# Optimization experiments

Hardware: AMD Instinct MI355X
Metric: run time of the kernel (lower is better)

The kernel has to match this reference:

```python
import jax, jax.numpy as jnp
import numpy as np

# ---- static config (from init_kwargs) ----
SAMPLE_RATE = 2048.0
MAX_SHIFT = int(0.025 * SAMPLE_RATE)          # 51 samples
NUM_BINS = 16
FFTLENGTH = 1.0                               # chisq_kernel_length (s)
DF = 1.0 / FFTLENGTH
NUM_FREQS = int(FFTLENGTH * SAMPLE_RATE // 2 + 1)   # 1025 == rfft bins of 2048 samples
HIGHPASS = 32.0
CHISQ_PENALTY = 1.0
_freqs = np.arange(NUM_FREQS) / FFTLENGTH
MASK = _freqs >= HIGHPASS                     # static numpy bool mask

BATCH, CHANNELS, DIM = 256, 2, 2048


def setup_inputs() -> dict:
    key = jax.random.key(0)
    k1, k2 = jax.random.split(key)
    x_hat = jax.random.normal(k1, (BATCH, CHANNELS, DIM), dtype=jnp.float32)
    x = jax.random.normal(k2, (BATCH, CHANNELS, DIM), dtype=jnp.float32)
    return {"x_hat": x_hat, "x": x}


def _center(x):
    xmin = x.min(-1, keepdims=True)
    xmax = x.max(-1, keepdims=True)
    return 2 * (x - xmin) / (xmax - xmin) - 1


def _shifted_pearson(x, y, max_shift):
    # x, y: [B, C, T]; returns corr: [W, B, C] with W = 2*max_shift + 1
    b, c, t = x.shape
    num_windows = 2 * max_shift + 1
    xp = jnp.pad(x, ((0, 0), (0, 0), (max_shift, max_shift)))
    # window w, position i -> xp[..., i + w]  (same layout as torch unfold)
    idx = jnp.arange(num_windows)[:, None] + jnp.arange(t)[None, :]   # [W, T]
    xw = xp[:, :, idx]                                                # [B, C, W, T]
    xw = jnp.transpose(xw, (2, 0, 1, 3))                              # [W, B, C, T]
    xw = xw - xw.mean(-1, keepdims=True)
    yc = y - y.mean(-1, keepdims=True)
    corr = (xw * yc).sum(-1)
    norm = (xw ** 2).sum(-1) * (yc ** 2).sum(-1)
    return corr / jnp.sqrt(norm)


def _snr_integral(a, b):
    # |4 * a * conj(b) * df| cumulatively summed over frequency
    integrand = a * jnp.conj(b)
    return jnp.abs(4 * integrand * DF).cumsum(-1)


def _chisq(htilde, stilde):
    htilde = htilde[:, :, MASK]
    stilde = stilde[:, :, MASK]
    # partition frequencies by the template's own optimal-SNR integral
    si = _snr_integral(htilde, htilde)                    # [B, C, F]
    total = si[:, :, -1:]
    bins = (jnp.arange(NUM_BINS + 1, dtype=si.dtype) / NUM_BINS) * total  # [B, C, NB+1]
    search = jax.vmap(jax.vmap(lambda a, v: jnp.searchsorted(a, v, side="right")))
    edges = search(si, bins)
    edges = jnp.clip(edges, 0, si.shape[-1] - 1)
    qtilde = htilde / jnp.sqrt(total).astype(htilde.dtype)
    # SNR per bin of the normalized template against the strain
    si2 = _snr_integral(qtilde, stilde)                   # [B, C, F]
    total2 = si2[:, :, -1:]
    right = jnp.take_along_axis(si2, edges[:, :, 1:], axis=-1)
    left = jnp.take_along_axis(si2, edges[:, :, :-1], axis=-1)
    snr_per_bin = right - left                            # [B, C, NB]
    summand = (snr_per_bin - total2 / NUM_BINS) ** 2
    chisq = NUM_BINS * summand.sum(-1) / (NUM_BINS - 1)
    return total2[:, :, 0], chisq


def reference(x_hat, x):
    x_hat = _center(x_hat)
    corr = _shifted_pearson(x_hat, x, MAX_SHIFT)          # [W, B, C]
    corr = corr.max(0)                                    # [B, C]
    loss = (1 - corr) / (1 + corr)
    htilde = jnp.fft.rfft(x_hat, axis=-1) / SAMPLE_RATE   # [B, C, 1025] complex
    stilde = jnp.fft.rfft(x, axis=-1) / SAMPLE_RATE
    _, chisq = _chisq(htilde, stilde)
    chisq = chisq * CHISQ_PENALTY
    loss = loss * (1 + chisq ** 3) ** (1.0 / 6.0)
    return loss
```

## Files before the change

### kernel.cpp

```cpp
#include <hip/hip_runtime.h>
#include <math.h>

#define ROWS 512
#define DIM 2048
#define MS 51
#define NWIN 103
#define KMIN 32
#define NMASK 993

__global__ __launch_bounds__(512) void fused_mfl_kernel(
    const float* __restrict__ xhat, const float* __restrict__ x,
    float* __restrict__ out)
{
    const int r = blockIdx.x;
    const int t = threadIdx.x;
    const int lane = t & 63;
    const int wave = t >> 6;

    __shared__ float smem[12928];
    float2* A2  = (float2*)smem;
    float2* B2  = (float2*)(smem + 4096);
    float2* TW  = (float2*)(smem + 8192);
    float* eArr = smem + 9216;
    float* gArr = smem + 10240;
    float* red6 = smem + 9216;
    float* ah   = smem + 12288;
    float* xhd  = smem + 12339;
    float* at_  = smem + 12390;
    float* xt_  = smem + 12441;
    float* Ah   = smem + 12492;
    float* Aqh  = smem + 12544;
    float* Xh   = smem + 12596;
    float* At   = smem + 12648;
    float* Aqt  = smem + 12700;
    float* Xt   = smem + 12752;
    float* corrv= smem + 12804;
    float* siA  = smem;
    float* siBr = smem + 1024;

    __shared__ float sc[8];
    __shared__ int   edges[17];
    __shared__ float summ[16];
    __shared__ float wsA[4], wsB[4];

    const float* xhp = xhat + (size_t)r * DIM;
    const float* xrp = x    + (size_t)r * DIM;
    float4 a4 = ((const float4*)xhp)[t];
    float4 b4 = ((const float4*)xrp)[t];
    float av[4] = {a4.x, a4.y, a4.z, a4.w};
    float bv[4] = {b4.x, b4.y, b4.z, b4.w};

    {
        float swv, cwv;
        sincosf((float)t * (-3.14159265358979323846f / 1024.0f), &swv, &cwv);
        TW[t] = make_float2(cwv, swv);
    }

#pragma unroll
    for (int j = 0; j < 4; ++j) {
        int i = 4 * t + j;
        A2[i] = make_float2(av[j], bv[j]);
        if (i < MS)        { ah[i] = av[j]; xhd[i] = bv[j]; }
        if (i >= DIM - MS) { at_[i-(DIM-MS)] = av[j]; xt_[i-(DIM-MS)] = bv[j]; }
    }
    {
        float mn4 = fminf(fminf(av[0],av[1]), fminf(av[2],av[3]));
        float mx4 = fmaxf(fmaxf(av[0],av[1]), fmaxf(av[2],av[3]));
        float sa = (av[0]+av[1])+(av[2]+av[3]);
        float qa = (av[0]*av[0]+av[1]*av[1])+(av[2]*av[2]+av[3]*av[3]);
        float sx = (bv[0]+bv[1])+(bv[2]+bv[3]);
        float qx = (bv[0]*bv[0]+bv[1]*bv[1])+(bv[2]*bv[2]+bv[3]*bv[3]);
        red6[t] = mn4; red6[512+t] = mx4; red6[1024+t] = sa;
        red6[1536+t] = qa; red6[2048+t] = sx; red6[2560+t] = qx;
    }
    __syncthreads();

    auto fft2048 = [&](const float2* Sp, float2* Dp, const int s) {
        const int q = t;
        const int u = q & ~(s - 1);
        float2 x0 = Sp[q], x1 = Sp[q+512], x2 = Sp[q+1024], x3 = Sp[q+1536];
        float t0r=x0.x+x2.x, t0i=x0.y+x2.y;
        float t1r=x0.x-x2.x, t1i=x0.y-x2.y;
        float t2r=x1.x+x3.x, t2i=x1.y+x3.y;
        float d3r=x1.x-x3.x, d3i=x1.y-x3.y;
        float t3r=d3i, t3i=-d3r;
        float2 w1 = TW[u];
        float w2r=w1.x*w1.x-w1.y*w1.y, w2i=2.f*w1.x*w1.y;
        float w3r=w2r*w1.x-w2i*w1.y,  w3i=w2r*w1.y+w2i*w1.x;
        float y0r=t0r+t2r, y0i=t0i+t2i;
        float a1r=t1r+t3r, a1i=t1i+t3i;
        float y1r=a1r*w1.x-a1i*w1.y, y1i=a1r*w1.y+a1i*w1.x;
        float a2r=t0r-t2r, a2i=t0i-t2i;
        float y2r=a2r*w2r-a2i*w2i, y2i=a2r*w2i+a2i*w2r;
        float a3r=t1r-t3r, a3i=t1i-t3i;
        float y3r=a3r*w3r-a3i*w3i, y3i=a3r*w3i+a3i*w3r;
        int base = q + 3*u;
        Dp[base]       = make_float2(y0r,y0i);
        Dp[base+s]     = make_float2(y1r,y1i);
        Dp[base+2*s]   = make_float2(y2r,y2i);
        Dp[base+3*s]   = make_float2(y3r,y3i);
    };
    auto fft1024 = [&](const float2* Sp, float2* Dp, const int s) {
        const int q = t;
        const int u = q & ~(s - 1);
        float2 x0 = Sp[q], x1 = Sp[q+256], x2 = Sp[q+512], x3 = Sp[q+768];
        float t0r=x0.x+x2.x, t0i=x0.y+x2.y;
        float t1r=x0.x-x2.x, t1i=x0.y-x2.y;
        float t2r=x1.x+x3.x, t2i=x1.y+x3.y;
        float d3r=x1.x-x3.x, d3i=x1.y-x3.y;
        float t3r=d3i, t3i=-d3r;
        float2 w1 = TW[2*u];
        float w2r=w1.x*w1.x-w1.y*w1.y, w2i=2.f*w1.x*w1.y;
        float w3r=w2r*w1.x-w2i*w1.y,  w3i=w2r*w1.y+w2i*w1.x;
        float y0r=t0r+t2r, y0i=t0i+t2i;
        float a1r=t1r+t3r, a1i=t1i+t3i;
        float y1r=a1r*w1.x-a1i*w1.y, y1i=a1r*w1.y+a1i*w1.x;
        float a2r=t0r-t2r, a2i=t0i-t2i;
        float y2r=a2r*w2r-a2i*w2i, y2i=a2r*w2i+a2i*w2r;
        float a3r=t1r-t3r, a3i=t1i-t3i;
        float y3r=a3r*w3r-a3i*w3i, y3i=a3r*w3i+a3i*w3r;
        int base = q + 3*u;
        Dp[base]       = make_float2(y0r,y0i);
        Dp[base+s]     = make_float2(y1r,y1i);
        Dp[base+2*s]   = make_float2(y2r,y2i);
        Dp[base+3*s]   = make_float2(y3r,y3i);
    };

    fft2048(A2, B2, 1);
    if (wave == 0) {
        float4 u, v;
        u=((const float4*)(red6     ))[2*lane]; v=((const float4*)(red6     ))[2*lane+1];
        float pmn=fminf(fminf(fminf(u.x,u.y),fminf(u.z,u.w)),fminf(fminf(v.x,v.y),fminf(v.z,v.w)));
        u=((const float4*)(red6+ 512))[2*lane]; v=((const float4*)(red6+ 512))[2*lane+1];
        float pmx=fmaxf(fmaxf(fmaxf(u.x,u.y),fmaxf(u.z,u.w)),fmaxf(fmaxf(v.x,v.y),fmaxf(v.z,v.w)));
        u=((const float4*)(red6+1024))[2*lane]; v=((const float4*)(red6+1024))[2*lane+1];
        float psa=((u.x+u.y)+(u.z+u.w))+((v.x+v.y)+(v.z+v.w));
        u=((const float4*)(red6+1536))[2*lane]; v=((const float4*)(red6+1536))[2*lane+1];
        float pqa=((u.x+u.y)+(u.z+u.w))+((v.x+v.y)+(v.z+v.w));
        u=((const float4*)(red6+2048))[2*lane]; v=((const float4*)(red6+2048))[2*lane+1];
        float psx=((u.x+u.y)+(u.z+u.w))+((v.x+v.y)+(v.z+v.w));
        u=((const float4*)(red6+2560))[2*lane]; v=((const float4*)(red6+2560))[2*lane+1];
        float pqx=((u.x+u.y)+(u.z+u.w))+((v.x+v.y)+(v.z+v.w));
#pragma unroll
        for (int d = 32; d; d >>= 1) {
            pmn=fminf(pmn,__shfl_down(pmn,d)); pmx=fmaxf(pmx,__shfl_down(pmx,d));
            psa+=__shfl_down(psa,d); pqa+=__shfl_down(pqa,d);
            psx+=__shfl_down(psx,d); pqx+=__shfl_down(pqx,d);
        }
        if (lane == 0) {
            float scl = 2.0f/(pmx - pmn);
            float Cc  = scl*pmn + 1.0f;
            float mean = psx * (1.0f/DIM);
            sc[0]=scl; sc[1]=Cc; sc[2]=mean; sc[3]=psa; sc[4]=pqa;
            sc[5]=pqx - (float)DIM*mean*mean;
        }
    }
    __syncthreads();

    fft2048(B2, A2, 4);
    if (wave == 2) {
        float va=0.f, vq=0.f, vx=0.f;
        if (lane >= 1 && lane <= MS) { float aa=ah[lane-1]; va=aa; vq=aa*aa; vx=xhd[lane-1]; }
#pragma unroll
        for (int d = 1; d < 64; d <<= 1) {
            float ya=__shfl_up(va,d), yq=__shfl_up(vq,d), yx=__shfl_up(vx,d);
            if (lane >= d) { va+=ya; vq+=yq; vx+=yx; }
        }
        if (lane <= MS) { Ah[lane]=va; Aqh[lane]=vq; Xh[lane]=vx; }
    } else if (wave == 3) {
        float va=0.f, vq=0.f, vx=0.f;
        if (lane >= 1 && lane <= MS) { float aa=at_[MS-lane]; va=aa; vq=aa*aa; vx=xt_[MS-lane]; }
#pragma unroll
        for (int d = 1; d < 64; d <<= 1) {
            float ya=__shfl_up(va,d), yq=__shfl_up(vq,d), yx=__shfl_up(vx,d);
            if (lane >= d) { va+=ya; vq+=yq; vx+=yx; }
        }
        if (lane <= MS) { At[lane]=va; Aqt[lane]=vq; Xt[lane]=vx; }
    }
    __syncthreads();
    fft2048(A2, B2, 16);  __syncthreads();
    fft2048(B2, A2, 64);  __syncthreads();
    fft2048(A2, B2, 256); __syncthreads();

    const float scl = sc[0], Cc = sc[1], mean = sc[2];
    const float Sa = sc[3], Qa = sc[4], Szz = sc[5];

    const float MSC = 0.5f * (1.0f / 2048.0f);
#pragma unroll
    for (int j = 0; j < 2; ++j) {
        int m = 2 * t + j;
        float e = 0.f, g = 0.f;
        if (m < NMASK) {
            int f = m + KMIN;
            float zfr, zfi;
            if (f < 1024) { float2 p=B2[f], q2=B2[f+1024]; zfr=p.x+q2.x; zfi=p.y+q2.y; }
            else          { float2 p=B2[0], q2=B2[1024];   zfr=p.x-q2.x; zfi=p.y-q2.y; }
            int gi = 2048 - f;
            float2 p2 = B2[gi-1024], q3 = B2[gi];
            float zgr = p2.x - q3.x, zgi = p2.y - q3.y;
            float hre = zfr + zgr, him = zfi - zgi;
            float sre = zfi + zgi, sim = zgr - zfr;
            float hm = scl * sqrtf(hre*hre + him*him) * MSC;
            float sm = sqrtf(sre*sre + sim*sim) * MSC;
            e = 4.f*hm*hm; g = 4.f*hm*sm;
            float pr = hre*sre + him*sim;
            float pi = him*sre - hre*sim;
            A2[f] = make_float2(pr, -pi);
            if (f < 1024) A2[2048-f] = make_float2(pr, pi);
        }
        eArr[m] = e; gArr[m] = g;
    }
    if (t < 32) {
        if (t == 0) A2[0] = make_float2(0.f, 0.f);
        else {
            int f = t;
            float2 p=B2[f], q2=B2[f+1024];
            float zfr=p.x+q2.x, zfi=p.y+q2.y;
            float2 p2=B2[1024-f], q3=B2[2048-f];
            float zgr=p2.x-q3.x, zgi=p2.y-q3.y;
            float hre=zfr+zgr, him=zfi-zgi;
            float sre=zfi+zgi, sim=zgr-zfr;
            float pr=hre*sre+him*sim, pi=him*sre-hre*sim;
            A2[f]=make_float2(pr,-pi);
            A2[2048-f]=make_float2(pr,pi);
        }
    }
    __syncthreads();

    float2* Qlo = B2;
    float2* Qhi = B2 + 1024;

    float se0=0,se1=0,se2=0,se3=0, sg0=0,sg1=0,sg2=0,sg3=0;
    float incE=0, incG=0, totE=0, totG=0;

    if (t < 256) {
        const int q = t;
        float2 wA = TW[q], wB = TW[q+256];
        auto mkQ = [&](int k, float2 w, int ni) -> float2 {
            float2 Pa = A2[k], Pb = A2[k+1024];
            float D1r = Pa.x+Pb.x, D1i = Pa.y+Pb.y;
            float D2r = Pa.x-Pb.x, D2i = Pa.y-Pb.y;
            float Er = D2r*w.x - D2i*w.y;
            float Ei = D2r*w.y + D2i*w.x;
            if (ni) return make_float2(D1r - Er, D1i - Ei);
            return make_float2(D1r + Ei, D1i - Er);
        };
        float2 x0 = mkQ(q,     wA, 0);
        float2 x1 = mkQ(q+256, wB, 0);
        float2 x2 = mkQ(q+512, wA, 1);
        float2 x3 = mkQ(q+768, wB, 1);
        float t0r=x0.x+x2.x, t0i=x0.y+x2.y;
        float t1r=x0.x-x2.x, t1i=x0.y-x2.y;
        float t2r=x1.x+x3.x, t2i=x1.y+x3.y;
        float d3r=x1.x-x3.x, d3i=x1.y-x3.y;
        float t3r=d3i, t3i=-d3r;
        float2 w1 = TW[2*q];
        float w2r=w1.x*w1.x-w1.y*w1.y, w2i=2.f*w1.x*w1.y;
        float w3r=w2r*w1.x-w2i*w1.y,  w3i=w2r*w1.y+w2i*w1.x;
        float y0r=t0r+t2r, y0i=t0i+t2i;
        float a1r=t1r+t3r, a1i=t1i+t3i;
        float y1r=a1r*w1.x-a1i*w1.y, y1i=a1r*w1.y+a1i*w1.x;
        float a2r=t0r-t2r, a2i=t0i-t2i;
        float y2r=a2r*w2r-a2i*w2i, y2i=a2r*w2i+a2i*w2r;
        float a3r=t1r-t3r, a3i=t1i-t3i;
        float y3r=a3r*w3r-a3i*w3i, y3i=a3r*w3i+a3i*w3r;
        Qlo[4*q]   = make_float2(y0r,y0i);
        Qlo[4*q+1] = make_float2(y1r,y1i);
        Qlo[4*q+2] = make_float2(y2r,y2i);
        Qlo[4*q+3] = make_float2(y3r,y3i);
    } else {
        int tt = t - 256;
        float4 e4 = ((const float4*)eArr)[tt];
        float4 g4 = ((const float4*)gArr)[tt];
        se0=e4.x; se1=se0+e4.y; se2=se1+e4.z; se3=se2+e4.w;
        sg0=g4.x; sg1=sg0+g4.y; sg2=sg1+g4.z; sg3=sg2+g4.w;
        totE=se3; totG=sg3; incE=totE; incG=totG;
#pragma unroll
        for (int d = 1; d < 64; d <<= 1) {
            float yE=__shfl_up(incE,d), yG=__shfl_up(incG,d);
            if (lane >= d) { incE+=yE; incG+=yG; }
        }
        if (lane == 63) { wsA[wave-4]=incE; wsB[wave-4]=incG; }
    }
    __syncthreads();

    if (t < 256) { fft1024(Qlo, Qhi, 4); }
    else {
        int tt = t - 256, w4 = wave - 4;
        float offE=0.f, offG=0.f;
        for (int w = 0; w < w4; ++w) { offE+=wsA[w]; offG+=wsB[w]; }
        float preE = offE + incE - totE;
        float preG = offG + incG - totG;
        ((float4*)siA)[tt]  = make_float4(preE+se0, preE+se1, preE+se2, preE+se3);
        ((float4*)siBr)[tt] = make_float4(preG+sg0, preG+sg1, preG+sg2, preG+sg3);
    }
    __syncthreads();

    if (t < 256) { fft1024(Qhi, Qlo, 16); }
    else if (t < 256 + 17) {
        int tl = t - 256;
        float total = siA[NMASK-1];
        float bin = ((float)tl * (1.0f/16.0f)) * total;
        int lo = 0, hi = NMASK;
        while (lo < hi) { int mid=(lo+hi)>>1; if (siA[mid] <= bin) lo=mid+1; else hi=mid; }
        edges[tl] = (lo < NMASK-1) ? lo : (NMASK-1);
    }
    __syncthreads();

    if (t < 256) { fft1024(Qlo, Qhi, 64); }
    else if (t < 256 + 16) {
        int tl = t - 256;
        float total = siA[NMASK-1];
        float qf = 1.0f / sqrtf(total);
        float total2 = siBr[NMASK-1] * qf;
        float snr = (siBr[edges[tl+1]] - siBr[edges[tl]]) * qf;
        float d = snr - total2 * (1.0f/16.0f);
        summ[tl] = d * d;
    }
    __syncthreads();

    if (t < 256) { fft1024(Qhi, Qlo, 256); }
    __syncthreads();

    if (t < 4 * NWIN) {
        int c = t >> 2, k = t & 3;
        int off = c - MS;
        float acc = 0.f;
        if (off > 0) {
            for (int j = k; j < off; j += 4) acc += ah[j] * (xt_[MS-off+j] - mean);
        } else if (off < 0) {
            int o = -off;
            for (int j = k; j < o; j += 4) acc += at_[MS-o+j] * (xhd[j] - mean);
        }
        acc += __shfl_down(acc, 1);
        acc += __shfl_down(acc, 2);
        if (k == 0) {
            int sidx = (off >= 0) ? off : (2048 + off);
            float2 Fv = Qlo[sidx >> 1];
            float val = (sidx & 1) ? -Fv.y : Fv.x;
            float circ = val * (1.0f/8192.0f);
            float Sin_a, Sin_q, Zex, nin;
            if (off >= 0) {
                Sin_a = Sa - Ah[off]; Sin_q = Qa - Aqh[off];
                Zex = Xt[off] - (float)off * mean; nin = 2048.0f - (float)off;
            } else {
                int o = -off;
                Sin_a = Sa - At[o]; Sin_q = Qa - Aqt[o];
                Zex = Xh[o] - (float)o * mean; nin = 2048.0f - (float)o;
            }
            float num = scl * (circ - acc) + Cc * Zex;
            float Sw  = scl * Sin_a - Cc * nin;
            float Sw2 = scl*scl*Sin_q - 2.f*scl*Cc*Sin_a + Cc*Cc*nin;
            float varw = Sw2 - Sw * Sw * (1.0f/2048.0f);
            corrv[c] = num / sqrtf(varw * Szz);
        }
    }
    __syncthreads();

    if (wave == 0) {
        float m = corrv[lane];
        if (lane + 64 < NWIN) m = fmaxf(m, corrv[lane + 64]);
#pragma unroll
        for (int d = 32; d; d >>= 1) m = fmaxf(m, __shfl_down(m, d));
        if (lane == 0) {
            float loss0 = (1.0f - m) / (1.0f + m);
            float ss = 0.f;
            for (int i = 0; i < 16; ++i) ss += summ[i];
            float chisq = 16.0f * ss / 15.0f;
            float c3 = chisq * chisq * chisq;
            out[r] = loss0 * powf(1.0f + c3, 1.0f/6.0f);
        }
    }
}

extern "C" void kernel_launch(void* const* d_in, const int* in_sizes, int n_in,
                              void* d_out, int out_size, void* d_ws, size_t ws_size,
                              hipStream_t stream) {
    const float* xhat = (const float*)d_in[0];
    const float* x    = (const float*)d_in[1];
    float* out = (float*)d_out;
    (void)in_sizes; (void)n_in; (void)out_size; (void)d_ws; (void)ws_size;

    fused_mfl_kernel<<<ROWS, 512, 0, stream>>>(xhat, x, out);
}
```

Before: 67.72 us.

## Fuse FFT stages with loads and spectrum pass to remove barriers

Performs the first radix-4 FFT stage in registers straight from strided global loads, which removes one shared-memory pass and one barrier. The spectrum product construction is folded into the inverse-FFT input twiddle, and the energy-bin computation moves into the upper waves that run alongside it. The last inverse FFT stage is evaluated only for the 103 needed lag outputs, and the edge-correction dot products are overlapped with the previous FFT stage. This cuts barriers and LDS traffic, at the cost of more complex indexing, uncoalesced scalar global loads, and duplicated spectrum arithmetic.

```diff
diff --git a/kernel.cpp b/kernel.cpp
--- a/kernel.cpp
+++ b/kernel.cpp
@@ -17,12 +17,14 @@
     const int lane = t & 63;
     const int wave = t >> 6;
 
-    __shared__ float smem[12928];
+    __shared__ float smem[13056];
     float2* A2  = (float2*)smem;
     float2* B2  = (float2*)(smem + 4096);
     float2* TW  = (float2*)(smem + 8192);
-    float* eArr = smem + 9216;
-    float* gArr = smem + 10240;
+    float2* Qlo = (float2*)smem;
+    float2* Qhi = (float2*)smem + 1024;
+    float* siA  = smem + 4096;
+    float* siBr = smem + 5120;
     float* red6 = smem + 9216;
     float* ah   = smem + 12288;
     float* xhd  = smem + 12339;
@@ -35,8 +37,7 @@
     float* Aqt  = smem + 12700;
     float* Xt   = smem + 12752;
     float* corrv= smem + 12804;
-    float* siA  = smem;
-    float* siBr = smem + 1024;
+    float* accv = smem + 12907;
 
     __shared__ float sc[8];
     __shared__ int   edges[17];
@@ -45,24 +46,13 @@
 
     const float* xhp = xhat + (size_t)r * DIM;
     const float* xrp = x    + (size_t)r * DIM;
-    float4 a4 = ((const float4*)xhp)[t];
-    float4 b4 = ((const float4*)xrp)[t];
-    float av[4] = {a4.x, a4.y, a4.z, a4.w};
-    float bv[4] = {b4.x, b4.y, b4.z, b4.w};
-
-    {
-        float swv, cwv;
-        sincosf((float)t * (-3.14159265358979323846f / 1024.0f), &swv, &cwv);
-        TW[t] = make_float2(cwv, swv);
-    }
-
-#pragma unroll
-    for (int j = 0; j < 4; ++j) {
-        int i = 4 * t + j;
-        A2[i] = make_float2(av[j], bv[j]);
-        if (i < MS)        { ah[i] = av[j]; xhd[i] = bv[j]; }
-        if (i >= DIM - MS) { at_[i-(DIM-MS)] = av[j]; xt_[i-(DIM-MS)] = bv[j]; }
-    }
+    float av[4] = {xhp[t], xhp[t+512], xhp[t+1024], xhp[t+1536]};
+    float bv[4] = {xrp[t], xrp[t+512], xrp[t+1024], xrp[t+1536]};
+
+    float swv, cwv;
+    sincosf((float)t * (-3.14159265358979323846f / 1024.0f), &swv, &cwv);
+    TW[t] = make_float2(cwv, swv);
+
     {
         float mn4 = fminf(fminf(av[0],av[1]), fminf(av[2],av[3]));
         float mx4 = fmaxf(fmaxf(av[0],av[1]), fmaxf(av[2],av[3]));
@@ -72,6 +62,29 @@
         float qx = (bv[0]*bv[0]+bv[1]*bv[1])+(bv[2]*bv[2]+bv[3]*bv[3]);
         red6[t] = mn4; red6[512+t] = mx4; red6[1024+t] = sa;
         red6[1536+t] = qa; red6[2048+t] = sx; red6[2560+t] = qx;
+    }
+    if (t < MS)   { ah[t] = av[0];      xhd[t] = bv[0]; }
+    if (t >= 461) { at_[t-461] = av[3]; xt_[t-461] = bv[3]; }
+    {
+        float t0r=av[0]+av[2], t0i=bv[0]+bv[2];
+        float t1r=av[0]-av[2], t1i=bv[0]-bv[2];
+        float t2r=av[1]+av[3], t2i=bv[1]+bv[3];
+        float d3r=av[1]-av[3], d3i=bv[1]-bv[3];
+        float t3r=d3i, t3i=-d3r;
+        float w1r=cwv, w1i=swv;
+        float w2r=w1r*w1r-w1i*w1i, w2i=2.f*w1r*w1i;
+        float w3r=w2r*w1r-w2i*w1i, w3i=w2r*w1i+w2i*w1r;
+        float y0r=t0r+t2r, y0i=t0i+t2i;
+        float a1r=t1r+t3r, a1i=t1i+t3i;
+        float y1r=a1r*w1r-a1i*w1i, y1i=a1r*w1i+a1i*w1r;
+        float a2r=t0r-t2r, a2i=t0i-t2i;
+        float y2r=a2r*w2r-a2i*w2i, y2i=a2r*w2i+a2i*w2r;
+        float a3r=t1r-t3r, a3i=t1i-t3i;
+        float y3r=a3r*w3r-a3i*w3i, y3i=a3r*w3i+a3i*w3r;
+        B2[4*t]   = make_float2(y0r,y0i);
+        B2[4*t+1] = make_float2(y1r,y1i);
+        B2[4*t+2] = make_float2(y2r,y2i);
+        B2[4*t+3] = make_float2(y3r,y3i);
     }
     __syncthreads();
 
@@ -95,10 +108,10 @@
         float a3r=t1r-t3r, a3i=t1i-t3i;
         float y3r=a3r*w3r-a3i*w3i, y3i=a3r*w3i+a3i*w3r;
         int base = q + 3*u;
-        Dp[base]       = make_float2(y0r,y0i);
-        Dp[base+s]     = make_float2(y1r,y1i);
-        Dp[base+2*s]   = make_float2(y2r,y2i);
-        Dp[base+3*s]   = make_float2(y3r,y3i);
+        Dp[base]     = make_float2(y0r,y0i);
+        Dp[base+s]   = make_float2(y1r,y1i);
+        Dp[base+2*s] = make_float2(y2r,y2i);
+        Dp[base+3*s] = make_float2(y3r,y3i);
     };
     auto fft1024 = [&](const float2* Sp, float2* Dp, const int s) {
         const int q = t;
@@ -120,13 +133,13 @@
         float a3r=t1r-t3r, a3i=t1i-t3i;
         float y3r=a3r*w3r-a3i*w3i, y3i=a3r*w3i+a3i*w3r;
         int base = q + 3*u;
-        Dp[base]       = make_float2(y0r,y0i);
-        Dp[base+s]     = make_float2(y1r,y1i);
-        Dp[base+2*s]   = make_float2(y2r,y2i);
-        Dp[base+3*s]   = make_float2(y3r,y3i);
+        Dp[base]     = make_float2(y0r,y0i);
+        Dp[base+s]   = make_float2(y1r,y1i);
+        Dp[base+2*s] = make_float2(y2r,y2i);
+        Dp[base+3*s] = make_float2(y3r,y3i);
     };
 
-    fft2048(A2, B2, 1);
+    fft2048(B2, A2, 4);
     if (wave == 0) {
         float4 u, v;
         u=((const float4*)(red6     ))[2*lane]; v=((const float4*)(red6     ))[2*lane+1];
@@ -154,11 +167,7 @@
             sc[0]=scl; sc[1]=Cc; sc[2]=mean; sc[3]=psa; sc[4]=pqa;
             sc[5]=pqx - (float)DIM*mean*mean;
         }
-    }
-    __syncthreads();
-
-    fft2048(B2, A2, 4);
-    if (wave == 2) {
+    } else if (wave == 2) {
         float va=0.f, vq=0.f, vx=0.f;
         if (lane >= 1 && lane <= MS) { float aa=ah[lane-1]; va=aa; vq=aa*aa; vx=xhd[lane-1]; }
 #pragma unroll
@@ -184,62 +193,37 @@
 
     const float scl = sc[0], Cc = sc[1], mean = sc[2];
     const float Sa = sc[3], Qa = sc[4], Szz = sc[5];
-
     const float MSC = 0.5f * (1.0f / 2048.0f);
-#pragma unroll
-    for (int j = 0; j < 2; ++j) {
-        int m = 2 * t + j;
-        float e = 0.f, g = 0.f;
-        if (m < NMASK) {
-            int f = m + KMIN;
-            float zfr, zfi;
-            if (f < 1024) { float2 p=B2[f], q2=B2[f+1024]; zfr=p.x+q2.x; zfi=p.y+q2.y; }
-            else          { float2 p=B2[0], q2=B2[1024];   zfr=p.x-q2.x; zfi=p.y-q2.y; }
-            int gi = 2048 - f;
-            float2 p2 = B2[gi-1024], q3 = B2[gi];
-            float zgr = p2.x - q3.x, zgi = p2.y - q3.y;
-            float hre = zfr + zgr, him = zfi - zgi;
-            float sre = zfi + zgi, sim = zgr - zfr;
-            float hm = scl * sqrtf(hre*hre + him*him) * MSC;
-            float sm = sqrtf(sre*sre + sim*sim) * MSC;
-            e = 4.f*hm*hm; g = 4.f*hm*sm;
-            float pr = hre*sre + him*sim;
-            float pi = him*sre - hre*sim;
-            A2[f] = make_float2(pr, -pi);
-            if (f < 1024) A2[2048-f] = make_float2(pr, pi);
-        }
-        eArr[m] = e; gArr[m] = g;
-    }
-    if (t < 32) {
-        if (t == 0) A2[0] = make_float2(0.f, 0.f);
-        else {
-            int f = t;
-            float2 p=B2[f], q2=B2[f+1024];
-            float zfr=p.x+q2.x, zfi=p.y+q2.y;
-            float2 p2=B2[1024-f], q3=B2[2048-f];
-            float zgr=p2.x-q3.x, zgi=p2.y-q3.y;
-            float hre=zfr+zgr, him=zfi-zgi;
-            float sre=zfi+zgi, sim=zgr-zfr;
-            float pr=hre*sre+him*sim, pi=him*sre-hre*sim;
-            A2[f]=make_float2(pr,-pi);
-            A2[2048-f]=make_float2(pr,pi);
-        }
-    }
-    __syncthreads();
-
-    float2* Qlo = B2;
-    float2* Qhi = B2 + 1024;
 
     float se0=0,se1=0,se2=0,se3=0, sg0=0,sg1=0,sg2=0,sg3=0;
     float incE=0, incG=0, totE=0, totG=0;
 
     if (t < 256) {
         const int q = t;
-        float2 wA = TW[q], wB = TW[q+256];
+        float2 wA = TW[q], wB = TW[q + 256];
         auto mkQ = [&](int k, float2 w, int ni) -> float2 {
-            float2 Pa = A2[k], Pb = A2[k+1024];
-            float D1r = Pa.x+Pb.x, D1i = Pa.y+Pb.y;
-            float D2r = Pa.x-Pb.x, D2i = Pa.y-Pb.y;
+            float2 Pa, Pb;
+            if (k == 0) {
+                float2 U = B2[0], V = B2[1024];
+                float drx = U.x - V.x, dry = U.y - V.y;
+                Pa = make_float2(0.f, 0.f);
+                Pb = make_float2(4.f * drx * dry, 0.f);
+            } else {
+                float2 U = B2[k], V = B2[k + 1024];
+                float2 R = B2[1024 - k], T = B2[2048 - k];
+                float zfr = U.x + V.x, zfi = U.y + V.y;
+                float zgr = R.x - T.x, zgi = R.y - T.y;
+                float hre = zfr + zgr, him = zfi - zgi;
+                float sre = zfi + zgi, sim = zgr - zfr;
+                Pa = make_float2(hre*sre + him*sim, -(him*sre - hre*sim));
+                float zfr2 = R.x + T.x, zfi2 = R.y + T.y;
+                float zgr2 = U.x - V.x, zgi2 = U.y - V.y;
+                float hre2 = zfr2 + zgr2, him2 = zfi2 - zgi2;
+                float sre2 = zfi2 + zgi2, sim2 = zgr2 - zfr2;
+                Pb = make_float2(hre2*sre2 + him2*sim2, him2*sre2 - hre2*sim2);
+            }
+            float D1r = Pa.x + Pb.x, D1i = Pa.y + Pb.y;
+            float D2r = Pa.x - Pb.x, D2i = Pa.y - Pb.y;
             float Er = D2r*w.x - D2i*w.y;
             float Ei = D2r*w.y + D2i*w.x;
             if (ni) return make_float2(D1r - Er, D1i - Ei);
@@ -270,10 +254,28 @@
         Qlo[4*q+3] = make_float2(y3r,y3i);
     } else {
         int tt = t - 256;
-        float4 e4 = ((const float4*)eArr)[tt];
-        float4 g4 = ((const float4*)gArr)[tt];
-        se0=e4.x; se1=se0+e4.y; se2=se1+e4.z; se3=se2+e4.w;
-        sg0=g4.x; sg1=sg0+g4.y; sg2=sg1+g4.z; sg3=sg2+g4.w;
+        float ee[4], gg[4];
+#pragma unroll
+        for (int j = 0; j < 4; ++j) {
+            int m = 4*tt + j;
+            ee[j] = 0.f; gg[j] = 0.f;
+            if (m < NMASK) {
+                int f = m + KMIN;
+                float zfr, zfi;
+                if (f < 1024) { float2 U=B2[f], V=B2[f+1024]; zfr=U.x+V.x; zfi=U.y+V.y; }
+                else          { float2 U=B2[0], V=B2[1024];   zfr=U.x-V.x; zfi=U.y-V.y; }
+                int gi = 2048 - f;
+                float2 p2 = B2[gi-1024], q3 = B2[gi];
+                float zgr = p2.x - q3.x, zgi = p2.y - q3.y;
+                float hre = zfr + zgr, him = zfi - zgi;
+                float sre = zfi + zgi, sim = zgr - zfr;
+                float hm = scl * sqrtf(hre*hre + him*him) * MSC;
+                float sm = sqrtf(sre*sre + sim*sim) * MSC;
+                ee[j] = 4.f*hm*hm; gg[j] = 4.f*hm*sm;
+            }
+        }
+        se0=ee[0]; se1=se0+ee[1]; se2=se1+ee[2]; se3=se2+ee[3];
+        sg0=gg[0]; sg1=sg0+gg[1]; sg2=sg1+gg[2]; sg3=sg2+gg[3];
         totE=se3; totG=sg3; incE=totE; incG=totG;
 #pragma unroll
         for (int d = 1; d < 64; d <<= 1) {
@@ -308,52 +310,64 @@
     __syncthreads();
 
     if (t < 256) { fft1024(Qlo, Qhi, 64); }
-    else if (t < 256 + 16) {
-        int tl = t - 256;
-        float total = siA[NMASK-1];
-        float qf = 1.0f / sqrtf(total);
-        float total2 = siBr[NMASK-1] * qf;
-        float snr = (siBr[edges[tl+1]] - siBr[edges[tl]]) * qf;
-        float d = snr - total2 * (1.0f/16.0f);
-        summ[tl] = d * d;
-    }
-    __syncthreads();
-
-    if (t < 256) { fft1024(Qhi, Qlo, 256); }
-    __syncthreads();
-
-    if (t < 4 * NWIN) {
-        int c = t >> 2, k = t & 3;
+    else {
+        int idx = t - 256;
+        if (idx < 16) {
+            float total = siA[NMASK-1];
+            float qf = 1.0f / sqrtf(total);
+            float total2 = siBr[NMASK-1] * qf;
+            float snr = (siBr[edges[idx+1]] - siBr[edges[idx]]) * qf;
+            float d = snr - total2 * (1.0f/16.0f);
+            summ[idx] = d * d;
+        }
+        int c = idx >> 1, k2 = idx & 1;
+        if (c < NWIN) {
+            int off = c - MS;
+            float acc = 0.f;
+            if (off > 0) {
+                for (int j = k2; j < off; j += 2) acc += ah[j] * (xt_[MS-off+j] - mean);
+            } else if (off < 0) {
+                int o = -off;
+                for (int j = k2; j < o; j += 2) acc += at_[MS-o+j] * (xhd[j] - mean);
+            }
+            acc += __shfl_down(acc, 1);
+            if (k2 == 0) accv[c] = acc;
+        }
+    }
+    __syncthreads();
+
+    if (t < NWIN) {
+        int c = t;
         int off = c - MS;
-        float acc = 0.f;
-        if (off > 0) {
-            for (int j = k; j < off; j += 4) acc += ah[j] * (xt_[MS-off+j] - mean);
-        } else if (off < 0) {
+        int sidx = (off >= 0) ? off : (2048 + off);
+        int n = sidx >> 1;
+        int q = n & 255;
+        float2 x0 = Qhi[q], x1 = Qhi[q+256], x2 = Qhi[q+512], x3 = Qhi[q+768];
+        float2 Fv;
+        if (n < 256) {
+            Fv = make_float2((x0.x+x2.x)+(x1.x+x3.x), (x0.y+x2.y)+(x1.y+x3.y));
+        } else {
+            float t1r_ = x0.x - x2.x, t1i_ = x0.y - x2.y;
+            float d3r_ = x1.x - x3.x, d3i_ = x1.y - x3.y;
+            Fv = make_float2(t1r_ - d3i_, t1i_ + d3r_);
+        }
+        float val = (sidx & 1) ? -Fv.y : Fv.x;
+        float circ = val * (1.0f/8192.0f);
+        float acc = accv[c];
+        float Sin_a, Sin_q, Zex, nin;
+        if (off >= 0) {
+            Sin_a = Sa - Ah[off]; Sin_q = Qa - Aqh[off];
+            Zex = Xt[off] - (float)off * mean; nin = 2048.0f - (float)off;
+        } else {
             int o = -off;
-            for (int j = k; j < o; j += 4) acc += at_[MS-o+j] * (xhd[j] - mean);
-        }
-        acc += __shfl_down(acc, 1);
-        acc += __shfl_down(acc, 2);
-        if (k == 0) {
-            int sidx = (off >= 0) ? off : (2048 + off);
-            float2 Fv = Qlo[sidx >> 1];
-            float val = (sidx & 1) ? -Fv.y : Fv.x;
-            float circ = val * (1.0f/8192.0f);
-            float Sin_a, Sin_q, Zex, nin;
-            if (off >= 0) {
-                Sin_a = Sa - Ah[off]; Sin_q = Qa - Aqh[off];
-                Zex = Xt[off] - (float)off * mean; nin = 2048.0f - (float)off;
-            } else {
-                int o = -off;
-                Sin_a = Sa - At[o]; Sin_q = Qa - Aqt[o];
-                Zex = Xh[o] - (float)o * mean; nin = 2048.0f - (float)o;
-            }
-            float num = scl * (circ - acc) + Cc * Zex;
-            float Sw  = scl * Sin_a - Cc * nin;
-            float Sw2 = scl*scl*Sin_q - 2.f*scl*Cc*Sin_a + Cc*Cc*nin;
-            float varw = Sw2 - Sw * Sw * (1.0f/2048.0f);
-            corrv[c] = num / sqrtf(varw * Szz);
-        }
+            Sin_a = Sa - At[o]; Sin_q = Qa - Aqt[o];
+            Zex = Xh[o] - (float)o * mean; nin = 2048.0f - (float)o;
+        }
+        float num = scl * (circ - acc) + Cc * Zex;
+        float Sw  = scl * Sin_a - Cc * nin;
+        float Sw2 = scl*scl*Sin_q - 2.f*scl*Cc*Sin_a + Cc*Cc*nin;
+        float varw = Sw2 - Sw * Sw * (1.0f/2048.0f);
+        corrv[c] = num / sqrtf(varw * Szz);
     }
     __syncthreads();
 
```

Result: no change. 67.23 us (-0.7%).
